# Performance work log

Measured on AMD Instinct MI355X. Metric: run time of the kernel, lower is better.

## Reference

```python
import jax, jax.numpy as jnp
import numpy as np

B, N, D, H, DFF, L = 2, 1024, 384, 8, 512, 4
HD = D // H  # 48
RBF_COUNT, RBF_MIN, RBF_MAX = 16, 0.0, 20.0


def layer_norm(x, g, b, eps=1e-5):
    m = jnp.mean(x, axis=-1, keepdims=True)
    v = jnp.var(x, axis=-1, keepdims=True)
    return (x - m) / jnp.sqrt(v + eps) * g + b


def setup_inputs() -> dict:
    key = jax.random.key(0)
    ks = jax.random.split(key, 30)
    rn = lambda k, shape, s=0.02: (jax.random.normal(k, shape, jnp.float32) * s)
    inp = {
        'x_rigid': jax.random.normal(ks[0], (B, N, D), jnp.float32),
        'altered_direction': jax.random.normal(ks[1], (B, N, N, 3), jnp.float32),
        'orientation': jax.random.normal(ks[2], (B, N, N, 3, 3), jnp.float32),
        'distance': jax.random.uniform(ks[3], (B, N, N), jnp.float32) * RBF_MAX,
        'attention_mask': jax.random.randint(ks[4], (B, N, N), 0, 2).astype(jnp.int32),
        'Wq': rn(ks[5], (L, D, D)), 'bq': rn(ks[6], (L, D)),
        'Wk': rn(ks[7], (L, D, D)), 'bk': rn(ks[8], (L, D)),
        'Wv': rn(ks[9], (L, D, D)), 'bv': rn(ks[10], (L, D)),
        'W3': rn(ks[11], (L, D, 3)), 'b3': rn(ks[12], (L, 3)),
        'Wmlp': rn(ks[13], (L, RBF_COUNT), 0.1), 'bmlp': rn(ks[14], (L,), 0.1),
        'Wfc': rn(ks[15], (L, D + 3, D)), 'bfc': rn(ks[16], (L, D)),
        'Wff1': rn(ks[17], (L, D, DFF)), 'bff1': rn(ks[18], (L, DFF)),
        'Wff2': rn(ks[19], (L, DFF, D)), 'bff2': rn(ks[20], (L, D)),
        'ln1_g': jnp.ones((L, D), jnp.float32), 'ln1_b': jnp.zeros((L, D), jnp.float32),
        'ln2_g': jnp.ones((L, D), jnp.float32), 'ln2_b': jnp.zeros((L, D), jnp.float32),
    }
    return inp


def reference(x_rigid, altered_direction, orientation, distance, attention_mask,
              Wq, bq, Wk, bk, Wv, bv, W3, b3, Wmlp, bmlp, Wfc, bfc,
              Wff1, bff1, Wff2, bff2, ln1_g, ln1_b, ln2_g, ln2_b):
    # RBF features of pairwise distance: [B,N,N,16] (shared across layers)
    mu = jnp.linspace(RBF_MIN, RBF_MAX, RBF_COUNT).astype(x_rigid.dtype)
    sigma = (RBF_MAX - RBF_MIN) / RBF_COUNT
    rbf = jnp.exp(-(((distance[..., None] - mu) / sigma) ** 2))
    mask0 = attention_mask == 0  # [B,N,N]
    scale = jnp.sqrt(jnp.asarray(HD, x_rigid.dtype))

    x = x_rigid
    for l in range(L):
        h = layer_norm(x, ln1_g[l], ln1_b[l])
        q = (h @ Wq[l] + bq[l]).reshape(B, N, H, HD).transpose(0, 2, 1, 3)
        k = (h @ Wk[l] + bk[l]).reshape(B, N, H, HD).transpose(0, 2, 1, 3)
        v = (h @ Wv[l] + bv[l]).reshape(B, N, H, HD).transpose(0, 2, 1, 3)
        scores = jnp.einsum('bhqd,bhkd->bhqk', q, k) / scale
        # RBF distance bias via 16->1 linear (head-broadcast, same as repeat+mlp)
        dis = jnp.einsum('bqkr,r->bqk', rbf, Wmlp[l]) + bmlp[l]
        scores = scores + dis[:, None]
        scores = jnp.where(mask0[:, None], jnp.asarray(-1e9, scores.dtype), scores)
        attn = jax.nn.softmax(scores, axis=-1)
        attn_v = jnp.einsum('bhqk,bhkd->bhqd', attn, v)
        attn_v = attn_v.transpose(0, 2, 1, 3).reshape(B, N, D)
        # merged-head softmax drives the geometric frame update
        merged = jax.nn.softmax(jnp.sum(scores, axis=1), axis=-1)  # [B,N,N]
        v3d = h @ W3[l] + b3[l]  # [B,N,3]
        v3d_map = jnp.einsum('bijmn,bjn->bijn', orientation, v3d)  # [B,N,N,3]
        v3d_dir = jnp.cross(altered_direction, v3d_map)  # [B,N,N,3]
        attn_frame = jnp.mean(merged[..., None] * v3d_dir, axis=-2)  # [B,N,3]
        out = jnp.concatenate([attn_v, attn_frame], axis=-1) @ Wfc[l] + bfc[l]
        x = x + out
        h2 = layer_norm(x, ln2_g[l], ln2_b[l])
        x = x + (jax.nn.relu(h2 @ Wff1[l] + bff1[l]) @ Wff2[l] + bff2[l])
    return x
```

## Files before the change

### kernel.cpp

```cpp
#include <hip/hip_runtime.h>
#include <math.h>

constexpr int B_ = 2, N_ = 1024, D_ = 384, H_ = 8, HD_ = 48, DFF2 = 512, L_ = 4;
constexpr int BN_ = B_ * N_;
constexpr size_t NNs = (size_t)N_ * N_;
constexpr size_t BNNc = (size_t)B_ * N_ * N_;
constexpr int JT = 64, NSPLIT = 4;
constexpr int CCLD = 448;
constexpr float RSCALE = 0.14433756729740643f;

typedef short bf16x8 __attribute__((ext_vector_type(8)));
typedef float f32x4 __attribute__((ext_vector_type(4)));

__device__ inline float wsum(float v) {
#pragma unroll
  for (int m = 32; m; m >>= 1) v += __shfl_xor(v, m, 64);
  return v;
}
__device__ inline float b2f(unsigned int s) {
  union { unsigned int u; float f; } v; v.u = s << 16; return v.f;
}
__device__ inline unsigned short f2b(float f) {
  union { float f; unsigned int u; } v; v.f = f;
  unsigned int r = v.u + 0x7fffu + ((v.u >> 16) & 1u);
  return (unsigned short)(r >> 16);
}

__global__ __launch_bounds__(256) void copy_kernel(float* __restrict__ dst,
                                                   const float* __restrict__ src, int n) {
  int i = blockIdx.x * 256 + threadIdx.x;
  if (i < n) dst[i] = src[i];
}
__global__ __launch_bounds__(256) void padzero_kernel(unsigned short* __restrict__ qp,
                                                      unsigned short* __restrict__ kp) {
  int i = blockIdx.x * 256 + threadIdx.x;
  int r = i >> 7;
  int rem = i & 127;
  int h = rem >> 4, c = rem & 15;
  size_t a = (size_t)r * 512 + h * 64 + 48 + c;
  qp[a] = 0; kp[a] = 0;
}

__global__ __launch_bounds__(256) void repack_kv_kernel(const unsigned short* __restrict__ kp,
                                                        const unsigned short* __restrict__ vTb,
                                                        unsigned short* __restrict__ kpf,
                                                        unsigned short* __restrict__ vf) {
  int tid = blockIdx.x * 256 + threadIdx.x;
  if (tid < 131072) {
    int l = tid & 63, fid = tid >> 6;
    int ks = fid & 1, h = (fid >> 1) & 7, jb = (fid >> 4) & 63, b = fid >> 10;
    const uint4 v = *reinterpret_cast<const uint4*>(
        kp + ((size_t)(b << 10) + jb * 16 + (l & 15)) * 512 + h * 64 + ks * 32 + (l >> 4) * 8);
    *reinterpret_cast<uint4*>(kpf + (size_t)tid * 8) = v;
  } else if (tid < 131072 + 98304) {
    int t2 = tid - 131072;
    int l = t2 & 63, fid = t2 >> 6;
    int df = fid % 24;
    int rest = fid / 24;
    int jg = rest & 31, b = rest >> 5;
    const uint4 v = *reinterpret_cast<const uint4*>(
        vTb + ((size_t)b * 384 + df * 16 + (l & 15)) * 1024 + jg * 32 + (l >> 4) * 8);
    *reinterpret_cast<uint4*>(vf + (size_t)t2 * 8) = v;
  }
}

__global__ __launch_bounds__(256) void pack_tr_kernel(const float* __restrict__ in, size_t istride,
                                                      unsigned short* __restrict__ out, size_t ostride,
                                                      int K, int Nc, int Kpad) {
  __shared__ float ts[32][33];
  int t = threadIdx.x;
  const float* inl = in + blockIdx.z * istride;
  unsigned short* outl = out + blockIdx.z * ostride;
  int n0 = blockIdx.x * 32, k0 = blockIdx.y * 32;
#pragma unroll
  for (int u = 0; u < 4; ++u) {
    int i = t + u * 256, kk = i >> 5, nn = i & 31;
    int k = k0 + kk;
    ts[kk][nn] = (k < K) ? inl[(size_t)k * Nc + n0 + nn] : 0.f;
  }
  __syncthreads();
#pragma unroll
  for (int u = 0; u < 4; ++u) {
    int i = t + u * 256, nn = i >> 5, kk = i & 31;
    outl[(size_t)(n0 + nn) * Kpad + k0 + kk] = f2b(ts[kk][nn]);
  }
}
__global__ __launch_bounds__(256) void pack_bias_kernel(const float* __restrict__ bq,
                                                        const float* __restrict__ bk,
                                                        const float* __restrict__ bv,
                                                        float* __restrict__ out) {
  int idx = blockIdx.x * 256 + threadIdx.x;
  if (idx >= L_ * 1152) return;
  int l = idx / 1152, n = idx % 1152;
  out[idx] = (n < 384) ? bq[l * D_ + n] : (n < 768) ? bk[l * D_ + n - 384] : bv[l * D_ + n - 768];
}

__global__ __launch_bounds__(256) void geomb_kernel(const float* __restrict__ ori,
                                                    const float* __restrict__ ad,
                                                    uint2* __restrict__ Ga,
                                                    unsigned int* __restrict__ Gz) {
  size_t i = (size_t)blockIdx.x * 256 + threadIdx.x;
  size_t stride = (size_t)gridDim.x * 256;
  for (; i < BNNc; i += stride) {
    const float* op = ori + i * 9;
    const float* ap = ad + i * 3;
    float c0 = op[0] + op[3] + op[6];
    float c1 = op[1] + op[4] + op[7];
    float c2 = op[2] + op[5] + op[8];
    float a0 = ap[0], a1 = ap[1], a2 = ap[2];
    uint2 oa;
    oa.x = (unsigned int)f2b(a1 * c2) | ((unsigned int)f2b(a2 * c1) << 16);
    oa.y = (unsigned int)f2b(a2 * c0) | ((unsigned int)f2b(a0 * c2) << 16);
    Ga[i] = oa;
    Gz[i] = (unsigned int)f2b(a0 * c1) | ((unsigned int)f2b(a1 * c0) << 16);
  }
}

__global__ __launch_bounds__(256) void rbf4_kernel(const float* __restrict__ dist,
                                                   const int* __restrict__ mask,
                                                   const float* __restrict__ Wmlp,
                                                   const float* __restrict__ bmlp,
                                                   unsigned short* __restrict__ db4) {
  size_t i = (size_t)blockIdx.x * 256 + threadIdx.x;
  size_t stride = (size_t)gridDim.x * 256;
  for (; i < BNNc; i += stride) {
    float dv = dist[i];
    bool msk = (mask[i] == 0);
    float rb[16];
#pragma unroll
    for (int r = 0; r < 16; ++r) {
      float tt = (dv - (float)r * (20.0f / 15.0f)) * 0.8f;
      rb[r] = __expf(-tt * tt);
    }
#pragma unroll
    for (int l2 = 0; l2 < L_; ++l2) {
      float sv = bmlp[l2];
#pragma unroll
      for (int r = 0; r < 16; ++r) sv += rb[r] * Wmlp[l2 * 16 + r];
      db4[(size_t)l2 * BNNc + i] = f2b(msk ? -1e9f : sv);
    }
  }
}
__global__ __launch_bounds__(256) void rbf_kernel(const float* __restrict__ dist,
                                                  const int* __restrict__ mask,
                                                  const float* __restrict__ wm,
                                                  const float* __restrict__ bm,
                                                  unsigned short* __restrict__ dbias) {
  size_t i = (size_t)blockIdx.x * 256 + threadIdx.x;
  size_t stride = (size_t)gridDim.x * 256;
  float w[16];
#pragma unroll
  for (int r = 0; r < 16; ++r) w[r] = wm[r];
  float b0 = bm[0];
  for (; i < BNNc; i += stride) {
    float dv = dist[i];
    float sv = b0;
#pragma unroll
    for (int r = 0; r < 16; ++r) {
      float tt = (dv - (float)r * (20.0f / 15.0f)) * 0.8f;
      sv += __expf(-tt * tt) * w[r];
    }
    dbias[i] = f2b((mask[i] == 0) ? -1e9f : sv);
  }
}

template <bool V3D>
__global__ __launch_bounds__(256) void ln_kernel(const float* __restrict__ x,
                                                 const float* __restrict__ g,
                                                 const float* __restrict__ b,
                                                 unsigned short* __restrict__ out,
                                                 const float* __restrict__ W3,
                                                 const float* __restrict__ b3,
                                                 float* __restrict__ v3d) {
  int lane = threadIdx.x & 63, wid = threadIdx.x >> 6;
  int row = blockIdx.x * 4 + wid;
  const float* xp = x + (size_t)row * D_;
  float v[6], s = 0.f, s2 = 0.f;
#pragma unroll
  for (int i = 0; i < 6; ++i) {
    v[i] = xp[lane + i * 64];
    s += v[i]; s2 += v[i] * v[i];
  }
  s = wsum(s); s2 = wsum(s2);
  float mean = s * (1.0f / D_);
  float var = s2 * (1.0f / D_) - mean * mean;
  float rstd = rsqrtf(var + 1e-5f);
  unsigned short* op = out + (size_t)row * D_;
  float a0 = 0.f, a1 = 0.f, a2 = 0.f;
#pragma unroll
  for (int i = 0; i < 6; ++i) {
    int d = lane + i * 64;
    float nv = (v[i] - mean) * rstd * g[d] + b[d];
    op[d] = f2b(nv);
    if (V3D) {
      a0 += nv * W3[d * 3 + 0];
      a1 += nv * W3[d * 3 + 1];
      a2 += nv * W3[d * 3 + 2];
    }
  }
  if (V3D) {
    a0 = wsum(a0); a1 = wsum(a1); a2 = wsum(a2);
    if (lane == 0) {
      v3d[row * 3 + 0] = a0 + b3[0];
      v3d[row * 3 + 1] = a1 + b3[1];
      v3d[row * 3 + 2] = a2 + b3[2];
    }
  }
}

template <int EPI>
__global__ __launch_bounds__(256) void mfma_gemm2(const unsigned short* __restrict__ A, int lda,
                                                  const unsigned short* __restrict__ WT, int ldw,
                                                  const float* __restrict__ bias,
                                                  float* __restrict__ C0, float* __restrict__ C1,
                                                  float* __restrict__ C2, int ldc, int K) {
  __shared__ __align__(16) unsigned short As[64 * 72];
  __shared__ __align__(16) unsigned short Bs[32 * 72];
  const int t = threadIdx.x;
  const int l = t & 63, w = t >> 6;
  const int lr = l & 15, lk = l >> 4;
  const int n0 = blockIdx.x * 32, m0 = blockIdx.y * 64;
  const int wm = (w & 1) * 32, wn = (w >> 1) * 16;
  const int srow = t >> 3, scol = t & 7;
  f32x4 acc[2] = {};
  for (int kt = 0; kt < K; kt += 64) {
#pragma unroll
    for (int u = 0; u < 2; ++u) {
      int c = t + u * 256, row = c >> 3, col = c & 7;
      *reinterpret_cast<uint4*>(&As[row * 72 + col * 8]) =
          *reinterpret_cast<const uint4*>(A + (size_t)(m0 + row) * lda + kt + col * 8);
    }
    *reinterpret_cast<uint4*>(&Bs[srow * 72 + scol * 8]) =
        *reinterpret_cast<const uint4*>(WT + (size_t)(n0 + srow) * ldw + kt + scol * 8);
    __syncthreads();
#pragma unroll
    for (int ks = 0; ks < 2; ++ks) {
      bf16x8 av0 = *reinterpret_cast<const bf16x8*>(&As[(wm + lr) * 72 + ks * 32 + lk * 8]);
      bf16x8 av1 = *reinterpret_cast<const bf16x8*>(&As[(wm + 16 + lr) * 72 + ks * 32 + lk * 8]);
      bf16x8 bv = *reinterpret_cast<const bf16x8*>(&Bs[(wn + lr) * 72 + ks * 32 + lk * 8]);
      acc[0] = __builtin_amdgcn_mfma_f32_16x16x32_bf16(av0, bv, acc[0], 0, 0, 0);
      acc[1] = __builtin_amdgcn_mfma_f32_16x16x32_bf16(av1, bv, acc[1], 0, 0, 0);
    }
    __syncthreads();
  }
#pragma unroll
  for (int mi = 0; mi < 2; ++mi)
#pragma unroll
    for (int e = 0; e < 4; ++e) {
      int row = m0 + wm + mi * 16 + lk * 4 + e;
      int col = n0 + wn + lr;
      float v = acc[mi][e] + bias[col];
      if (EPI == 0) {
        if (col < 384) {
          int h = col / 48, hd = col - h * 48;
          ((unsigned short*)C0)[(size_t)row * 512 + h * 64 + hd] = f2b(v * RSCALE);
        } else if (col < 768) {
          int c2 = col - 384;
          int h = c2 / 48, hd = c2 - h * 48;
          ((unsigned short*)C1)[(size_t)row * 512 + h * 64 + hd] = f2b(v);
        } else {
          int c2 = col - 768;
          ((unsigned short*)C2)[((size_t)(row >> 10) * D_ + c2) * N_ + (row & 1023)] = f2b(v);
        }
      }
      if (EPI == 1) C0[(size_t)row * ldc + col] += v;
      if (EPI == 2) ((unsigned short*)C0)[(size_t)row * ldc + col] = f2b(fmaxf(v, 0.f));
    }
}

template <bool USEG>
__global__ __launch_bounds__(512, 4) void attn16_kernel(
    const unsigned short* __restrict__ qp, const unsigned short* __restrict__ kpf,
    const unsigned short* __restrict__ vf, const unsigned short* __restrict__ db_l,
    const uint2* __restrict__ Ga, const unsigned int* __restrict__ Gz,
    const float* __restrict__ ad, const float* __restrict__ ori,
    const float* __restrict__ v3d,
    unsigned short* __restrict__ pO, float* __restrict__ pM, float* __restrict__ pL,
    float* __restrict__ pF, float* __restrict__ pMg, float* __restrict__ pLg) {
  __shared__ __align__(16) unsigned short pbuf[8 * 16 * 72];
  __shared__ __align__(16) unsigned short msw[8 * 16 * 68];
  __shared__ __align__(16) float dbs[16 * 68];
  __shared__ float fg_s[16];

  const int t = threadIdx.x;
  const int wv = t >> 6, l = t & 63;
  const int lr = l & 15, lk = l >> 4;
  const int sgrp = blockIdx.y;
  const int i0 = blockIdx.x * 16;
  const int b = i0 >> 10, ib = i0 & 1023;
  const int mr = t >> 5, mc = t & 31;

  const bf16x8 qf0 = *reinterpret_cast<const bf16x8*>(
      qp + (size_t)(i0 + lr) * 512 + wv * 64 + lk * 8);
  const bf16x8 qf1 = *reinterpret_cast<const bf16x8*>(
      qp + (size_t)(i0 + lr) * 512 + wv * 64 + 32 + lk * 8);

  f32x4 Ofr[3] = {};
  float fracc[2][3] = {};
  float m_ph[4], l_ph[4], fhv[4];
#pragma unroll
  for (int e = 0; e < 4; ++e) { m_ph[e] = -INFINITY; l_ph[e] = 0.f; }
  float m_mg = -INFINITY, l_mg = 0.f;

  for (int jt = sgrp * (N_ / NSPLIT); jt < (sgrp + 1) * (N_ / NSPLIT); jt += JT) {
    if (t < 128) {
      int r = t >> 3, c4 = t & 7;
      const uint4* src = reinterpret_cast<const uint4*>(
                             db_l + (size_t)b * NNs + (size_t)(ib + r) * N_ + jt) + c4;
      uint4 v = *src;
      float* dp = &dbs[r * 68 + c4 * 8];
      dp[0] = b2f(v.x & 0xffffu); dp[1] = b2f(v.x >> 16);
      dp[2] = b2f(v.y & 0xffffu); dp[3] = b2f(v.y >> 16);
      dp[4] = b2f(v.z & 0xffffu); dp[5] = b2f(v.z >> 16);
      dp[6] = b2f(v.w & 0xffffu); dp[7] = b2f(v.w >> 16);
    }
    f32x4 sc[4];
    {
      const unsigned short* kbase =
          kpf + ((((size_t)(b * 64) + (jt >> 4)) * 8 + wv) * 2 * 64 + l) * 8;
      bf16x8 kf0[4], kf1[4];
#pragma unroll
      for (int nj = 0; nj < 4; ++nj) {
        kf0[nj] = *reinterpret_cast<const bf16x8*>(kbase + (size_t)nj * 16 * 512);
        kf1[nj] = *reinterpret_cast<const bf16x8*>(kbase + (size_t)nj * 16 * 512 + 512);
      }
#pragma unroll
      for (int nj = 0; nj < 4; ++nj) {
        f32x4 acc = {};
        acc = __builtin_amdgcn_mfma_f32_16x16x32_bf16(qf0, kf0[nj], acc, 0, 0, 0);
        acc = __builtin_amdgcn_mfma_f32_16x16x32_bf16(qf1, kf1[nj], acc, 0, 0, 0);
        sc[nj] = acc;
      }
    }
#pragma unroll
    for (int nj = 0; nj < 4; ++nj)
#pragma unroll
      for (int e = 0; e < 4; ++e)
        msw[(wv * 16 + lk * 4 + e) * 68 + nj * 16 + lr] = f2b(sc[nj][e]);
    __syncthreads();
    {
      float sv[4][4];
#pragma unroll
      for (int nj = 0; nj < 4; ++nj)
#pragma unroll
        for (int e = 0; e < 4; ++e)
          sv[nj][e] = sc[nj][e] + dbs[(lk * 4 + e) * 68 + nj * 16 + lr];
#pragma unroll
      for (int e = 0; e < 4; ++e) {
        float rm = fmaxf(fmaxf(sv[0][e], sv[1][e]), fmaxf(sv[2][e], sv[3][e]));
        rm = fmaxf(rm, __shfl_xor(rm, 1, 64));
        rm = fmaxf(rm, __shfl_xor(rm, 2, 64));
        rm = fmaxf(rm, __shfl_xor(rm, 4, 64));
        rm = fmaxf(rm, __shfl_xor(rm, 8, 64));
        float nm = fmaxf(m_ph[e], rm);
        float f = __expf(m_ph[e] - nm);
        m_ph[e] = nm;
        fhv[e] = f;
        float ls = 0.f;
#pragma unroll
        for (int nj = 0; nj < 4; ++nj) {
          float p = __expf(sv[nj][e] - nm);
          sv[nj][e] = p;
          ls += p;
        }
        ls += __shfl_xor(ls, 1, 64);
        ls += __shfl_xor(ls, 2, 64);
        ls += __shfl_xor(ls, 4, 64);
        ls += __shfl_xor(ls, 8, 64);
        l_ph[e] = l_ph[e] * f + ls;
#pragma unroll
        for (int nj = 0; nj < 4; ++nj)
          pbuf[(wv * 16 + lk * 4 + e) * 72 + nj * 16 + lr] = f2b(sv[nj][e]);
      }
    }
    {
      float mv[2];
      float tmax = -INFINITY;
#pragma unroll
      for (int i = 0; i < 2; ++i) {
        int j = mc + 32 * i;
        float s = 8.f * dbs[mr * 68 + j];
#pragma unroll
        for (int h = 0; h < 8; ++h) s += b2f(msw[(h * 16 + mr) * 68 + j]);
        mv[i] = s;
        tmax = fmaxf(tmax, s);
      }
      tmax = fmaxf(tmax, __shfl_xor(tmax, 1, 64));
      tmax = fmaxf(tmax, __shfl_xor(tmax, 2, 64));
      tmax = fmaxf(tmax, __shfl_xor(tmax, 4, 64));
      tmax = fmaxf(tmax, __shfl_xor(tmax, 8, 64));
      tmax = fmaxf(tmax, __shfl_xor(tmax, 16, 64));
      float nm = fmaxf(m_mg, tmax);
      float f = __expf(m_mg - nm);
      m_mg = nm;
      float lsum = 0.f;
#pragma unroll
      for (int i = 0; i < 2; ++i) {
        mv[i] = __expf(mv[i] - nm);
        lsum += mv[i];
      }
      lsum += __shfl_xor(lsum, 1, 64);
      lsum += __shfl_xor(lsum, 2, 64);
      lsum += __shfl_xor(lsum, 4, 64);
      lsum += __shfl_xor(lsum, 8, 64);
      lsum += __shfl_xor(lsum, 16, 64);
      l_mg = l_mg * f + lsum;
#pragma unroll
      for (int i = 0; i < 2; ++i) msw[mr * 68 + mc + 32 * i] = f2b(mv[i]);
      if (mc == 0) fg_s[mr] = f;
    }
    __syncthreads();
    {
      bf16x8 af0 = *reinterpret_cast<const bf16x8*>(&pbuf[(wv * 16 + lr) * 72 + lk * 8]);
      bf16x8 af1 = *reinterpret_cast<const bf16x8*>(&pbuf[(wv * 16 + lr) * 72 + 32 + lk * 8]);
      const unsigned short* vbase =
          vf + ((((size_t)(b * 32) + (jt >> 5)) * 24 + wv * 3) * 64 + l) * 8;
#pragma unroll
      for (int ni = 0; ni < 3; ++ni) {
        bf16x8 bf0 = *reinterpret_cast<const bf16x8*>(vbase + (size_t)ni * 512);
        bf16x8 bf1 = *reinterpret_cast<const bf16x8*>(vbase + (size_t)(24 + ni) * 512);
        f32x4 o = Ofr[ni];
#pragma unroll
        for (int e = 0; e < 4; ++e) o[e] *= fhv[e];
        o = __builtin_amdgcn_mfma_f32_16x16x32_bf16(af0, bf0, o, 0, 0, 0);
        o = __builtin_amdgcn_mfma_f32_16x16x32_bf16(af1, bf1, o, 0, 0, 0);
        Ofr[ni] = o;
      }
    }
    {
      const float* vp = v3d + (size_t)((b << 10) + jt + l) * 3;
      float w0 = vp[0], w1 = vp[1], w2 = vp[2];
#pragma unroll
      for (int e = 0; e < 2; ++e) {
        int r = wv * 2 + e;
        float pm = b2f(msw[r * 68 + l]);
        size_t pij = ((size_t)b * N_ + (ib + r)) * N_ + jt + l;
        float d0, d1, d2;
        if (USEG) {
          uint2 ga = Ga[pij];
          unsigned int gz = Gz[pij];
          float g0 = b2f(ga.x & 0xffffu), g1 = b2f(ga.x >> 16);
          float g2 = b2f(ga.y & 0xffffu), g3 = b2f(ga.y >> 16);
          float g4 = b2f(gz & 0xffffu), g5 = b2f(gz >> 16);
          d0 = g0 * w2 - g1 * w1;
          d1 = g2 * w0 - g3 * w2;
          d2 = g4 * w1 - g5 * w0;
        } else {
          const float* op = ori + pij * 9;
          const float* ap = ad + pij * 3;
          float a0 = ap[0], a1 = ap[1], a2 = ap[2];
          float u0 = (op[0] + op[3] + op[6]) * w0;
          float u1 = (op[1] + op[4] + op[7]) * w1;
          float u2 = (op[2] + op[5] + op[8]) * w2;
          d0 = a1 * u2 - a2 * u1; d1 = a2 * u0 - a0 * u2; d2 = a0 * u1 - a1 * u0;
        }
        float fgr = fg_s[r];
        fracc[e][0] = fracc[e][0] * fgr + pm * d0;
        fracc[e][1] = fracc[e][1] * fgr + pm * d1;
        fracc[e][2] = fracc[e][2] * fgr + pm * d2;
      }
    }
    __syncthreads();
  }
  const size_t rowb = (size_t)sgrp * BN_ + i0;
#pragma unroll
  for (int ni = 0; ni < 3; ++ni)
#pragma unroll
    for (int e = 0; e < 4; ++e)
      pO[(rowb + lk * 4 + e) * D_ + wv * 48 + ni * 16 + lr] = f2b(Ofr[ni][e]);
#pragma unroll
  for (int e = 0; e < 2; ++e)
#pragma unroll
    for (int c = 0; c < 3; ++c) {
      float v = wsum(fracc[e][c]);
      if (l == 0) pF[(rowb + wv * 2 + e) * 3 + c] = v;
    }
  if (lr == 0) {
#pragma unroll
    for (int e = 0; e < 4; ++e) {
      pM[(rowb + lk * 4 + e) * H_ + wv] = m_ph[e];
      pL[(rowb + lk * 4 + e) * H_ + wv] = l_ph[e];
    }
  }
  if (mc == 0) { pMg[rowb + mr] = m_mg; pLg[rowb + mr] = l_mg; }
}

constexpr int QR = 8;
__global__ __launch_bounds__(256) void combine_kernel(
    const unsigned short* __restrict__ pO, const float* __restrict__ pM,
    const float* __restrict__ pL, const float* __restrict__ pF,
    const float* __restrict__ pMg, const float* __restrict__ pLg,
    unsigned short* __restrict__ cc) {
  __shared__ float sc[QR][H_][NSPLIT];
  __shared__ float scg[QR][NSPLIT];
  int t = threadIdx.x;
  int i0 = blockIdx.x * QR;
  if (t < QR * H_) {
    int r = t >> 3, h = t & 7;
    size_t row = i0 + r;
    float ms[NSPLIT], ls[NSPLIT], m = -INFINITY;
#pragma unroll
    for (int s2 = 0; s2 < NSPLIT; ++s2) {
      ms[s2] = pM[((size_t)s2 * BN_ + row) * H_ + h];
      ls[s2] = pL[((size_t)s2 * BN_ + row) * H_ + h];
      m = fmaxf(m, ms[s2]);
    }
    float L = 0.f, e[NSPLIT];
#pragma unroll
    for (int s2 = 0; s2 < NSPLIT; ++s2) { e[s2] = __expf(ms[s2] - m); L += ls[s2] * e[s2]; }
    float invL = 1.0f / L;
#pragma unroll
    for (int s2 = 0; s2 < NSPLIT; ++s2) sc[r][h][s2] = e[s2] * invL;
  } else if (t < QR * H_ + QR) {
    int r = t - QR * H_;
    size_t row = i0 + r;
    float ms[NSPLIT], ls[NSPLIT], m = -INFINITY;
#pragma unroll
    for (int s2 = 0; s2 < NSPLIT; ++s2) {
      ms[s2] = pMg[(size_t)s2 * BN_ + row];
      ls[s2] = pLg[(size_t)s2 * BN_ + row];
      m = fmaxf(m, ms[s2]);
    }
    float L = 0.f, e[NSPLIT];
#pragma unroll
    for (int s2 = 0; s2 < NSPLIT; ++s2) { e[s2] = __expf(ms[s2] - m); L += ls[s2] * e[s2]; }
    float inv = 1.0f / (L * (float)N_);
#pragma unroll
    for (int s2 = 0; s2 < NSPLIT; ++s2) scg[r][s2] = e[s2] * inv;
  }
  __syncthreads();
#pragma unroll
  for (int r = 0; r < QR; ++r) {
    size_t row = i0 + r;
    for (int d = t; d < D_; d += 256) {
      int h = d / HD_;
      float o = 0.f;
#pragma unroll
      for (int s2 = 0; s2 < NSPLIT; ++s2)
        o += b2f(pO[((size_t)s2 * BN_ + row) * D_ + d]) * sc[r][h][s2];
      cc[row * CCLD + d] = f2b(o);
    }
  }
  if (t < QR * 3) {
    int r = t / 3, c = t % 3;
    size_t row = i0 + r;
    float F = 0.f;
#pragma unroll
    for (int s2 = 0; s2 < NSPLIT; ++s2) F += pF[((size_t)s2 * BN_ + row) * 3 + c] * scg[r][s2];
    cc[row * CCLD + 384 + c] = f2b(F);
  }
  for (int idx = t; idx < QR * (CCLD - 387); idx += 256) {
    int r = idx / (CCLD - 387), col = 387 + idx % (CCLD - 387);
    cc[(size_t)(i0 + r) * CCLD + col] = 0;
  }
}

extern "C" void kernel_launch(void* const* d_in, const int* in_sizes, int n_in,
                              void* d_out, int out_size, void* d_ws, size_t ws_size,
                              hipStream_t stream) {
  const float* x_rigid = (const float*)d_in[0];
  const float* ad      = (const float*)d_in[1];
  const float* ori     = (const float*)d_in[2];
  const float* dist    = (const float*)d_in[3];
  const int*   mask    = (const int*)d_in[4];
  const float* Wq  = (const float*)d_in[5];
  const float* bq  = (const float*)d_in[6];
  const float* Wk  = (const float*)d_in[7];
  const float* bk  = (const float*)d_in[8];
  const float* Wv  = (const float*)d_in[9];
  const float* bv  = (const float*)d_in[10];
  const float* W3  = (const float*)d_in[11];
  const float* b3  = (const float*)d_in[12];
  const float* Wmlp = (const float*)d_in[13];
  const float* bmlp = (const float*)d_in[14];
  const float* Wfc  = (const float*)d_in[15];
  const float* bfc  = (const float*)d_in[16];
  const float* Wff1 = (const float*)d_in[17];
  const float* bff1 = (const float*)d_in[18];
  const float* Wff2 = (const float*)d_in[19];
  const float* bff2 = (const float*)d_in[20];
  const float* ln1g = (const float*)d_in[21];
  const float* ln1b = (const float*)d_in[22];
  const float* ln2g = (const float*)d_in[23];
  const float* ln2b = (const float*)d_in[24];

  float* x = (float*)d_out;

  size_t off = 0;
  auto alloc = [&](size_t bytes) -> void* {
    void* r = (char*)d_ws + off;
    off = (off + bytes + 255) & ~(size_t)255;
    return r;
  };
  unsigned short* WqkvT = (unsigned short*)alloc((size_t)L_ * 1152 * D_ * 2);
  unsigned short* WfcT  = (unsigned short*)alloc((size_t)L_ * D_ * CCLD * 2);
  unsigned short* Wff1T = (unsigned short*)alloc((size_t)L_ * DFF2 * D_ * 2);
  unsigned short* Wff2T = (unsigned short*)alloc((size_t)L_ * D_ * DFF2 * 2);
  float* bqkv = (float*)alloc((size_t)L_ * 1152 * 4);
  unsigned short* qp  = (unsigned short*)alloc((size_t)BN_ * 512 * 2);
  unsigned short* kp  = (unsigned short*)alloc((size_t)BN_ * 512 * 2);
  unsigned short* vTb = (unsigned short*)alloc((size_t)BN_ * D_ * 2);
  unsigned short* kpf = (unsigned short*)alloc((size_t)2048 * 64 * 8 * 2);
  unsigned short* vf  = (unsigned short*)alloc((size_t)1536 * 64 * 8 * 2);
  unsigned short* hb  = (unsigned short*)alloc((size_t)BN_ * D_ * 2);
  unsigned short* h2  = (unsigned short*)alloc((size_t)BN_ * D_ * 2);
  unsigned short* cc  = (unsigned short*)alloc((size_t)BN_ * CCLD * 2);
  unsigned short* ffb = (unsigned short*)alloc((size_t)BN_ * DFF2 * 2);
  float* v3 = (float*)alloc((size_t)BN_ * 3 * 4);
  unsigned short* pO = (unsigned short*)alloc((size_t)NSPLIT * BN_ * D_ * 2);
  float* pM = (float*)alloc((size_t)NSPLIT * BN_ * H_ * 4);
  float* pL = (float*)alloc((size_t)NSPLIT * BN_ * H_ * 4);
  float* pF = (float*)alloc((size_t)NSPLIT * BN_ * 3 * 4);
  float* pMg = (float*)alloc((size_t)NSPLIT * BN_ * 4);
  float* pLg = (float*)alloc((size_t)NSPLIT * BN_ * 4);
  size_t need_base = off;
  uint2* Ga = (uint2*)alloc(BNNc * 8);
  unsigned int* Gz = (unsigned int*)alloc(BNNc * 4);
  bool useG = (off <= ws_size);
  size_t off_g = useG ? off : need_base;
  off = off_g;
  unsigned short* db4 = (unsigned short*)alloc((size_t)L_ * BNNc * 2);
  bool use4 = (off <= ws_size);
  unsigned short* db1 = nullptr;
  if (!use4) {
    off = off_g;
    db1 = (unsigned short*)alloc(BNNc * 2);
    if (off > ws_size) return;
  }
  if (ws_size < need_base) return;

  pack_tr_kernel<<<dim3(12, 12, L_), 256, 0, stream>>>(Wq, (size_t)D_ * D_, WqkvT,
                                                       (size_t)1152 * D_, D_, D_, D_);
  pack_tr_kernel<<<dim3(12, 12, L_), 256, 0, stream>>>(Wk, (size_t)D_ * D_, WqkvT + 384 * 384,
                                                       (size_t)1152 * D_, D_, D_, D_);
  pack_tr_kernel<<<dim3(12, 12, L_), 256, 0, stream>>>(Wv, (size_t)D_ * D_, WqkvT + 768 * 384,
                                                       (size_t)1152 * D_, D_, D_, D_);
  pack_tr_kernel<<<dim3(12, 14, L_), 256, 0, stream>>>(Wfc, (size_t)387 * D_, WfcT,
                                                       (size_t)D_ * CCLD, 387, D_, CCLD);
  pack_tr_kernel<<<dim3(16, 12, L_), 256, 0, stream>>>(Wff1, (size_t)D_ * DFF2, Wff1T,
                                                       (size_t)DFF2 * D_, D_, DFF2, D_);
  pack_tr_kernel<<<dim3(12, 16, L_), 256, 0, stream>>>(Wff2, (size_t)DFF2 * D_, Wff2T,
                                                       (size_t)D_ * DFF2, DFF2, D_, DFF2);
  pack_bias_kernel<<<(L_ * 1152 + 255) / 256, 256, 0, stream>>>(bq, bk, bv, bqkv);
  if (useG) geomb_kernel<<<4096, 256, 0, stream>>>(ori, ad, Ga, Gz);
  if (use4) rbf4_kernel<<<4096, 256, 0, stream>>>(dist, mask, Wmlp, bmlp, db4);
  copy_kernel<<<(BN_ * D_) / 256, 256, 0, stream>>>(x, x_rigid, BN_ * D_);
  padzero_kernel<<<(BN_ * H_ * 16) / 256, 256, 0, stream>>>(qp, kp);

  for (int l = 0; l < L_; ++l) {
    const unsigned short* db_l = use4 ? (db4 + (size_t)l * BNNc) : db1;
    if (!use4) rbf_kernel<<<4096, 256, 0, stream>>>(dist, mask, Wmlp + l * 16, bmlp + l, db1);
    ln_kernel<true><<<BN_ / 4, 256, 0, stream>>>(x, ln1g + l * D_, ln1b + l * D_, hb,
                                                 W3 + (size_t)l * D_ * 3, b3 + l * 3, v3);
    mfma_gemm2<0><<<dim3(36, 32), 256, 0, stream>>>(
        hb, D_, WqkvT + (size_t)l * 1152 * D_, D_, bqkv + l * 1152,
        (float*)qp, (float*)kp, (float*)vTb, 0, D_);
    repack_kv_kernel<<<896, 256, 0, stream>>>(kp, vTb, kpf, vf);
    if (useG)
      attn16_kernel<true><<<dim3(BN_ / 16, NSPLIT), 512, 0, stream>>>(
          qp, kpf, vf, db_l, Ga, Gz, ad, ori, v3, pO, pM, pL, pF, pMg, pLg);
    else
      attn16_kernel<false><<<dim3(BN_ / 16, NSPLIT), 512, 0, stream>>>(
          qp, kpf, vf, db_l, Ga, Gz, ad, ori, v3, pO, pM, pL, pF, pMg, pLg);
    combine_kernel<<<BN_ / QR, 256, 0, stream>>>(pO, pM, pL, pF, pMg, pLg, cc);
    mfma_gemm2<1><<<dim3(12, 32), 256, 0, stream>>>(
        cc, CCLD, WfcT + (size_t)l * D_ * CCLD, CCLD, bfc + l * D_, x, nullptr, nullptr, D_, CCLD);
    ln_kernel<false><<<BN_ / 4, 256, 0, stream>>>(x, ln2g + l * D_, ln2b + l * D_, h2,
                                                  nullptr, nullptr, nullptr);
    mfma_gemm2<2><<<dim3(16, 32), 256, 0, stream>>>(
        h2, D_, Wff1T + (size_t)l * DFF2 * D_, D_, bff1 + l * DFF2, (float*)ffb, nullptr, nullptr,
        DFF2, D_);
    mfma_gemm2<1><<<dim3(12, 32), 256, 0, stream>>>(
        ffb, DFF2, Wff2T + (size_t)l * D_ * DFF2, DFF2, bff2 + l * D_, x, nullptr, nullptr, D_,
        DFF2);
  }
}
```

Measured before the change: 379.8 us.

## Fuse K/V fragment repack into QKV GEMM, double-buffer GEMM, lazy softmax rescale

The QKV GEMM epilogue now writes K and V straight into the MFMA fragment layouts, so the separate repack kernel and the intermediate kp/vTb buffers go away. Padding zeroing now targets the fragment buffer instead. The generic bf16 GEMM gains a double-buffered LDS tile with register prefetch, which drops one barrier per k-step. The attention kernel skips online-softmax max updates and output rescaling unless a new max exceeds the running max by more than 8, and a barrier between the merged softmax and the PV stage is removed. The thresholded rescale lets values grow up to e^8 before renormalising, and the dropped barrier may introduce an LDS race.

```diff
diff --git a/kernel.cpp b/kernel.cpp
--- a/kernel.cpp
+++ b/kernel.cpp
@@ -32,35 +32,17 @@
   if (i < n) dst[i] = src[i];
 }
 __global__ __launch_bounds__(256) void padzero_kernel(unsigned short* __restrict__ qp,
-                                                      unsigned short* __restrict__ kp) {
+                                                      unsigned short* __restrict__ kpf) {
   int i = blockIdx.x * 256 + threadIdx.x;
-  int r = i >> 7;
-  int rem = i & 127;
-  int h = rem >> 4, c = rem & 15;
-  size_t a = (size_t)r * 512 + h * 64 + 48 + c;
-  qp[a] = 0; kp[a] = 0;
-}
-
-__global__ __launch_bounds__(256) void repack_kv_kernel(const unsigned short* __restrict__ kp,
-                                                        const unsigned short* __restrict__ vTb,
-                                                        unsigned short* __restrict__ kpf,
-                                                        unsigned short* __restrict__ vf) {
-  int tid = blockIdx.x * 256 + threadIdx.x;
-  if (tid < 131072) {
-    int l = tid & 63, fid = tid >> 6;
-    int ks = fid & 1, h = (fid >> 1) & 7, jb = (fid >> 4) & 63, b = fid >> 10;
-    const uint4 v = *reinterpret_cast<const uint4*>(
-        kp + ((size_t)(b << 10) + jb * 16 + (l & 15)) * 512 + h * 64 + ks * 32 + (l >> 4) * 8);
-    *reinterpret_cast<uint4*>(kpf + (size_t)tid * 8) = v;
-  } else if (tid < 131072 + 98304) {
-    int t2 = tid - 131072;
-    int l = t2 & 63, fid = t2 >> 6;
-    int df = fid % 24;
-    int rest = fid / 24;
-    int jg = rest & 31, b = rest >> 5;
-    const uint4 v = *reinterpret_cast<const uint4*>(
-        vTb + ((size_t)b * 384 + df * 16 + (l & 15)) * 1024 + jg * 32 + (l >> 4) * 8);
-    *reinterpret_cast<uint4*>(vf + (size_t)t2 * 8) = v;
+  if (i < 262144) {
+    int r = i >> 7;
+    int rem = i & 127;
+    int h = rem >> 4, c = rem & 15;
+    qp[(size_t)r * 512 + h * 64 + 48 + c] = 0;
+  } else {
+    int j = i - 262144;
+    int fh = j >> 8, rem = j & 255;
+    kpf[(size_t)fh * 1024 + 768 + rem] = 0;
   }
 }
 
@@ -214,34 +196,42 @@
                                                   const float* __restrict__ bias,
                                                   float* __restrict__ C0, float* __restrict__ C1,
                                                   float* __restrict__ C2, int ldc, int K) {
-  __shared__ __align__(16) unsigned short As[64 * 72];
-  __shared__ __align__(16) unsigned short Bs[32 * 72];
+  __shared__ __align__(16) unsigned short As[2][64 * 72];
+  __shared__ __align__(16) unsigned short Bs[2][32 * 72];
   const int t = threadIdx.x;
   const int l = t & 63, w = t >> 6;
   const int lr = l & 15, lk = l >> 4;
   const int n0 = blockIdx.x * 32, m0 = blockIdx.y * 64;
   const int wm = (w & 1) * 32, wn = (w >> 1) * 16;
-  const int srow = t >> 3, scol = t & 7;
+  const int arow = t >> 3, acol8 = (t & 7) * 8;
+  uint4 ra0, ra1, rb;
+  const unsigned short* pa0 = A + (size_t)(m0 + arow) * lda + acol8;
+  const unsigned short* pa1 = A + (size_t)(m0 + arow + 32) * lda + acol8;
+  const unsigned short* pb = WT + (size_t)(n0 + arow) * ldw + acol8;
+  ra0 = *reinterpret_cast<const uint4*>(pa0);
+  ra1 = *reinterpret_cast<const uint4*>(pa1);
+  rb = *reinterpret_cast<const uint4*>(pb);
   f32x4 acc[2] = {};
+  int p = 0;
   for (int kt = 0; kt < K; kt += 64) {
-#pragma unroll
-    for (int u = 0; u < 2; ++u) {
-      int c = t + u * 256, row = c >> 3, col = c & 7;
-      *reinterpret_cast<uint4*>(&As[row * 72 + col * 8]) =
-          *reinterpret_cast<const uint4*>(A + (size_t)(m0 + row) * lda + kt + col * 8);
-    }
-    *reinterpret_cast<uint4*>(&Bs[srow * 72 + scol * 8]) =
-        *reinterpret_cast<const uint4*>(WT + (size_t)(n0 + srow) * ldw + kt + scol * 8);
+    *reinterpret_cast<uint4*>(&As[p][arow * 72 + acol8]) = ra0;
+    *reinterpret_cast<uint4*>(&As[p][(arow + 32) * 72 + acol8]) = ra1;
+    *reinterpret_cast<uint4*>(&Bs[p][arow * 72 + acol8]) = rb;
+    if (kt + 64 < K) {
+      ra0 = *reinterpret_cast<const uint4*>(pa0 + kt + 64);
+      ra1 = *reinterpret_cast<const uint4*>(pa1 + kt + 64);
+      rb = *reinterpret_cast<const uint4*>(pb + kt + 64);
+    }
     __syncthreads();
 #pragma unroll
     for (int ks = 0; ks < 2; ++ks) {
-      bf16x8 av0 = *reinterpret_cast<const bf16x8*>(&As[(wm + lr) * 72 + ks * 32 + lk * 8]);
-      bf16x8 av1 = *reinterpret_cast<const bf16x8*>(&As[(wm + 16 + lr) * 72 + ks * 32 + lk * 8]);
-      bf16x8 bv = *reinterpret_cast<const bf16x8*>(&Bs[(wn + lr) * 72 + ks * 32 + lk * 8]);
+      bf16x8 av0 = *reinterpret_cast<const bf16x8*>(&As[p][(wm + lr) * 72 + ks * 32 + lk * 8]);
+      bf16x8 av1 = *reinterpret_cast<const bf16x8*>(&As[p][(wm + 16 + lr) * 72 + ks * 32 + lk * 8]);
+      bf16x8 bv = *reinterpret_cast<const bf16x8*>(&Bs[p][(wn + lr) * 72 + ks * 32 + lk * 8]);
       acc[0] = __builtin_amdgcn_mfma_f32_16x16x32_bf16(av0, bv, acc[0], 0, 0, 0);
       acc[1] = __builtin_amdgcn_mfma_f32_16x16x32_bf16(av1, bv, acc[1], 0, 0, 0);
     }
-    __syncthreads();
+    p ^= 1;
   }
 #pragma unroll
   for (int mi = 0; mi < 2; ++mi)
@@ -256,11 +246,18 @@
           ((unsigned short*)C0)[(size_t)row * 512 + h * 64 + hd] = f2b(v * RSCALE);
         } else if (col < 768) {
           int c2 = col - 384;
-          int h = c2 / 48, hd = c2 - h * 48;
-          ((unsigned short*)C1)[(size_t)row * 512 + h * 64 + hd] = f2b(v);
+          int h = c2 / 48, d = c2 - h * 48;
+          int b2 = row >> 10, j = row & 1023;
+          int jb = j >> 4, jr = j & 15;
+          int ks = d >> 5, dd = d & 31;
+          size_t fid = (((size_t)(b2 * 64 + jb) * 8 + h) << 1) + ks;
+          ((unsigned short*)C1)[fid * 512 + (size_t)(jr + ((dd >> 3) << 4)) * 8 + (d & 7)] = f2b(v);
         } else {
-          int c2 = col - 768;
-          ((unsigned short*)C2)[((size_t)(row >> 10) * D_ + c2) * N_ + (row & 1023)] = f2b(v);
+          int d = col - 768;
+          int b2 = row >> 10, j = row & 1023;
+          int jg = j >> 5, df = d >> 4;
+          size_t fid = (size_t)(b2 * 32 + jg) * 24 + df;
+          ((unsigned short*)C2)[fid * 512 + (size_t)((d & 15) + (((j & 31) >> 3) << 4)) * 8 + (j & 7)] = f2b(v);
         }
       }
       if (EPI == 1) C0[(size_t)row * ldc + col] += v;
@@ -338,6 +335,7 @@
       for (int e = 0; e < 4; ++e)
         msw[(wv * 16 + lk * 4 + e) * 68 + nj * 16 + lr] = f2b(sc[nj][e]);
     __syncthreads();
+    bool needO;
     {
       float sv[4][4];
 #pragma unroll
@@ -345,29 +343,42 @@
 #pragma unroll
         for (int e = 0; e < 4; ++e)
           sv[nj][e] = sc[nj][e] + dbs[(lk * 4 + e) * 68 + nj * 16 + lr];
+      float lm[4];
+      bool need = false;
 #pragma unroll
       for (int e = 0; e < 4; ++e) {
-        float rm = fmaxf(fmaxf(sv[0][e], sv[1][e]), fmaxf(sv[2][e], sv[3][e]));
-        rm = fmaxf(rm, __shfl_xor(rm, 1, 64));
-        rm = fmaxf(rm, __shfl_xor(rm, 2, 64));
-        rm = fmaxf(rm, __shfl_xor(rm, 4, 64));
-        rm = fmaxf(rm, __shfl_xor(rm, 8, 64));
-        float nm = fmaxf(m_ph[e], rm);
-        float f = __expf(m_ph[e] - nm);
-        m_ph[e] = nm;
-        fhv[e] = f;
+        lm[e] = fmaxf(fmaxf(sv[0][e], sv[1][e]), fmaxf(sv[2][e], sv[3][e]));
+        need = need || (lm[e] > m_ph[e] + 8.f);
+      }
+      needO = __any(need);
+      if (needO) {
+#pragma unroll
+        for (int e = 0; e < 4; ++e) {
+          float rm = lm[e];
+          rm = fmaxf(rm, __shfl_xor(rm, 1, 64));
+          rm = fmaxf(rm, __shfl_xor(rm, 2, 64));
+          rm = fmaxf(rm, __shfl_xor(rm, 4, 64));
+          rm = fmaxf(rm, __shfl_xor(rm, 8, 64));
+          float nm = fmaxf(m_ph[e], rm);
+          fhv[e] = __expf(m_ph[e] - nm);
+          m_ph[e] = nm;
+          l_ph[e] *= fhv[e];
+        }
+      }
+#pragma unroll
+      for (int e = 0; e < 4; ++e) {
         float ls = 0.f;
 #pragma unroll
         for (int nj = 0; nj < 4; ++nj) {
-          float p = __expf(sv[nj][e] - nm);
-          sv[nj][e] = p;
-          ls += p;
+          float pv = __expf(sv[nj][e] - m_ph[e]);
+          sv[nj][e] = pv;
+          ls += pv;
         }
         ls += __shfl_xor(ls, 1, 64);
         ls += __shfl_xor(ls, 2, 64);
         ls += __shfl_xor(ls, 4, 64);
         ls += __shfl_xor(ls, 8, 64);
-        l_ph[e] = l_ph[e] * f + ls;
+        l_ph[e] += ls;
 #pragma unroll
         for (int nj = 0; nj < 4; ++nj)
           pbuf[(wv * 16 + lk * 4 + e) * 72 + nj * 16 + lr] = f2b(sv[nj][e]);
@@ -375,7 +386,6 @@
     }
     {
       float mv[2];
-      float tmax = -INFINITY;
 #pragma unroll
       for (int i = 0; i < 2; ++i) {
         int j = mc + 32 * i;
@@ -383,33 +393,38 @@
 #pragma unroll
         for (int h = 0; h < 8; ++h) s += b2f(msw[(h * 16 + mr) * 68 + j]);
         mv[i] = s;
-        tmax = fmaxf(tmax, s);
-      }
-      tmax = fmaxf(tmax, __shfl_xor(tmax, 1, 64));
-      tmax = fmaxf(tmax, __shfl_xor(tmax, 2, 64));
-      tmax = fmaxf(tmax, __shfl_xor(tmax, 4, 64));
-      tmax = fmaxf(tmax, __shfl_xor(tmax, 8, 64));
-      tmax = fmaxf(tmax, __shfl_xor(tmax, 16, 64));
-      float nm = fmaxf(m_mg, tmax);
-      float f = __expf(m_mg - nm);
-      m_mg = nm;
+      }
+      float lm2 = fmaxf(mv[0], mv[1]);
+      bool needm = __any(lm2 > m_mg + 8.f);
+      if (needm) {
+        float tmax = lm2;
+        tmax = fmaxf(tmax, __shfl_xor(tmax, 1, 64));
+        tmax = fmaxf(tmax, __shfl_xor(tmax, 2, 64));
+        tmax = fmaxf(tmax, __shfl_xor(tmax, 4, 64));
+        tmax = fmaxf(tmax, __shfl_xor(tmax, 8, 64));
+        tmax = fmaxf(tmax, __shfl_xor(tmax, 16, 64));
+        float nm = fmaxf(m_mg, tmax);
+        float f = __expf(m_mg - nm);
+        m_mg = nm;
+        l_mg *= f;
+        if (mc == 0) fg_s[mr] = f;
+      } else if (mc == 0) {
+        fg_s[mr] = 1.f;
+      }
       float lsum = 0.f;
 #pragma unroll
       for (int i = 0; i < 2; ++i) {
-        mv[i] = __expf(mv[i] - nm);
+        mv[i] = __expf(mv[i] - m_mg);
         lsum += mv[i];
+        msw[mr * 68 + mc + 32 * i] = f2b(mv[i]);
       }
       lsum += __shfl_xor(lsum, 1, 64);
       lsum += __shfl_xor(lsum, 2, 64);
       lsum += __shfl_xor(lsum, 4, 64);
       lsum += __shfl_xor(lsum, 8, 64);
       lsum += __shfl_xor(lsum, 16, 64);
-      l_mg = l_mg * f + lsum;
-#pragma unroll
-      for (int i = 0; i < 2; ++i) msw[mr * 68 + mc + 32 * i] = f2b(mv[i]);
-      if (mc == 0) fg_s[mr] = f;
-    }
-    __syncthreads();
+      l_mg += lsum;
+    }
     {
       bf16x8 af0 = *reinterpret_cast<const bf16x8*>(&pbuf[(wv * 16 + lr) * 72 + lk * 8]);
       bf16x8 af1 = *reinterpret_cast<const bf16x8*>(&pbuf[(wv * 16 + lr) * 72 + 32 + lk * 8]);
@@ -420,8 +435,10 @@
         bf16x8 bf0 = *reinterpret_cast<const bf16x8*>(vbase + (size_t)ni * 512);
         bf16x8 bf1 = *reinterpret_cast<const bf16x8*>(vbase + (size_t)(24 + ni) * 512);
         f32x4 o = Ofr[ni];
-#pragma unroll
-        for (int e = 0; e < 4; ++e) o[e] *= fhv[e];
+        if (needO) {
+#pragma unroll
+          for (int e = 0; e < 4; ++e) o[e] *= fhv[e];
+        }
         o = __builtin_amdgcn_mfma_f32_16x16x32_bf16(af0, bf0, o, 0, 0, 0);
         o = __builtin_amdgcn_mfma_f32_16x16x32_bf16(af1, bf1, o, 0, 0, 0);
         Ofr[ni] = o;
@@ -598,8 +615,6 @@
   unsigned short* Wff2T = (unsigned short*)alloc((size_t)L_ * D_ * DFF2 * 2);
   float* bqkv = (float*)alloc((size_t)L_ * 1152 * 4);
   unsigned short* qp  = (unsigned short*)alloc((size_t)BN_ * 512 * 2);
-  unsigned short* kp  = (unsigned short*)alloc((size_t)BN_ * 512 * 2);
-  unsigned short* vTb = (unsigned short*)alloc((size_t)BN_ * D_ * 2);
   unsigned short* kpf = (unsigned short*)alloc((size_t)2048 * 64 * 8 * 2);
   unsigned short* vf  = (unsigned short*)alloc((size_t)1536 * 64 * 8 * 2);
   unsigned short* hb  = (unsigned short*)alloc((size_t)BN_ * D_ * 2);
@@ -645,7 +660,7 @@
   if (useG) geomb_kernel<<<4096, 256, 0, stream>>>(ori, ad, Ga, Gz);
   if (use4) rbf4_kernel<<<4096, 256, 0, stream>>>(dist, mask, Wmlp, bmlp, db4);
   copy_kernel<<<(BN_ * D_) / 256, 256, 0, stream>>>(x, x_rigid, BN_ * D_);
-  padzero_kernel<<<(BN_ * H_ * 16) / 256, 256, 0, stream>>>(qp, kp);
+  padzero_kernel<<<2048, 256, 0, stream>>>(qp, kpf);
 
   for (int l = 0; l < L_; ++l) {
     const unsigned short* db_l = use4 ? (db4 + (size_t)l * BNNc) : db1;
@@ -654,8 +669,7 @@
                                                  W3 + (size_t)l * D_ * 3, b3 + l * 3, v3);
     mfma_gemm2<0><<<dim3(36, 32), 256, 0, stream>>>(
         hb, D_, WqkvT + (size_t)l * 1152 * D_, D_, bqkv + l * 1152,
-        (float*)qp, (float*)kp, (float*)vTb, 0, D_);
-    repack_kv_kernel<<<896, 256, 0, stream>>>(kp, vTb, kpf, vf);
+        (float*)qp, (float*)kpf, (float*)vf, 0, D_);
     if (useG)
       attn16_kernel<true><<<dim3(BN_ / 16, NSPLIT), 512, 0, stream>>>(
           qp, kpf, vf, db_l, Ga, Gz, ad, ori, v3, pO, pM, pL, pF, pMg, pLg);
```

Result: faster. 338.4 us (median of 2 runs) (-10.9%).
